# Kernel optimization log

Hardware: AMD Instinct MI355X
Metric: run time of the kernel (lower is better)

Reference implementation:

```python
import jax, jax.numpy as jnp
import numpy as np

B, T, D, H = 4, 2048, 512, 8
K = D // H  # head dim = 64

def setup_inputs() -> dict:
    key = jax.random.key(0)
    k1, k2, k3, k4 = jax.random.split(key, 4)
    x = jax.random.normal(k1, (B, T, D), dtype=jnp.float32)
    # torch nn.Linear stores weight as [out_features, in_features]
    w_qkv = jax.random.normal(k2, (3 * D, D), dtype=jnp.float32) * (D ** -0.5)
    w_proj = jax.random.normal(k3, (D, D), dtype=jnp.float32) * (D ** -0.5)
    b_proj = jax.random.normal(k4, (D,), dtype=jnp.float32) * 0.01
    return {"x": x, "w_qkv": w_qkv, "w_proj": w_proj, "b_proj": b_proj}

def reference(x, w_qkv, w_proj, b_proj):
    Bx, Tx, Dx = x.shape
    # qkv projection (no bias): [B,T,3D]
    qkv = jnp.einsum('btd,ed->bte', x, w_qkv)
    q, k, v = jnp.split(qkv, 3, axis=-1)
    # [B,H,T,K]
    def heads(t):
        return t.reshape(Bx, Tx, H, K).transpose(0, 2, 1, 3)
    q, k, v = heads(q), heads(k), heads(v)
    # scaled scores with causal mask
    scores = jnp.einsum('bhqk,bhsk->bhqs', q, k) * (K ** -0.5)  # [B,H,T,T]
    causal = jnp.tril(jnp.ones((Tx, Tx), dtype=bool))
    scores = jnp.where(causal, scores, -jnp.inf)
    attn = jax.nn.softmax(scores, axis=-1)  # dropout p=0.0 -> identity
    out = jnp.einsum('bhqs,bhsk->bhqk', attn, v)  # [B,H,T,K]
    out = out.transpose(0, 2, 1, 3).reshape(Bx, Tx, Dx)
    out = jnp.einsum('btd,ed->bte', out, w_proj) + b_proj
    return out
```

## Files before the change

### kernel.cpp

```cpp
#include <hip/hip_runtime.h>
#include <hip/hip_bf16.h>


typedef unsigned short u16;
typedef __attribute__((ext_vector_type(8))) __bf16 bf16x8;
typedef __attribute__((ext_vector_type(8))) unsigned short u16x8;
typedef __attribute__((ext_vector_type(4))) float f32x4;
typedef __attribute__((ext_vector_type(4))) unsigned u32x4;

#define DEV static __device__ __forceinline__

DEV void async16(const u16* g, u16* l) {
  __builtin_amdgcn_global_load_lds(
      (const __attribute__((address_space(1))) unsigned int*)g,
      (__attribute__((address_space(3))) unsigned int*)l, 16, 0, 0);
}
DEV u16x8 gld8(const u16* p) { return *(const u16x8*)p; }
DEV void lst8(u16* p, u16x8 v) { *(u16x8*)p = v; }
DEV bf16x8 ldsld8(const u16* p) {
  return __builtin_bit_cast(bf16x8, *(const u16x8*)p);
}
DEV f32x4 mfma16(bf16x8 a, bf16x8 b, f32x4 c) {
  return __builtin_amdgcn_mfma_f32_16x16x32_bf16(a, b, c, 0, 0, 0);
}
DEV u16 f2b(float f) {
  unsigned u = __builtin_bit_cast(unsigned, f);
  u += 0x7FFFu + ((u >> 16) & 1u);
  return (u16)(u >> 16);
}
DEV unsigned pk2(float x, float y) {
  __hip_bfloat162 t = __float22bfloat162_rn(float2{x, y});
  unsigned r;
  __builtin_memcpy(&r, &t, 4);
  return r;
}
DEV u16x8 pack8(f32x4 a, f32x4 b) {
  u32x4 t;
  t[0] = pk2(a[0], a[1]);
  t[1] = pk2(a[2], a[3]);
  t[2] = pk2(b[0], b[1]);
  t[3] = pk2(b[2], b[3]);
  return __builtin_bit_cast(u16x8, t);
}

__global__ void cvt_all(const float* __restrict__ x, const float* __restrict__ wq,
                        u16* __restrict__ xb, u16* __restrict__ wqb) {
  constexpr long NX = 8192L * 512 / 8;
  constexpr long NQ = 1536L * 512 / 8;
  const long i = (long)blockIdx.x * 256 + threadIdx.x;
  if (i < NX) {
    const float* p = x + i * 8;
    *(u16x8*)(xb + i * 8) = pack8(*(const f32x4*)p, *(const f32x4*)(p + 4));
  } else if (i < NX + NQ) {
    const long j = i - NX;
    const float* p = wq + j * 8;
    *(u16x8*)(wqb + j * 8) = pack8(*(const f32x4*)p, *(const f32x4*)(p + 4));
  }
}

__global__ void gemm_bb(const u16* __restrict__ A, const u16* __restrict__ Bt,
                        u16* __restrict__ C, int N, int K) {
  __shared__ __align__(16) u16 As[2][128 * 32];
  __shared__ __align__(16) u16 Bs[2][128 * 32];

  const int t = threadIdx.x, lane = t & 63, w = t >> 6;
  const int lane15 = lane & 15, quad = lane >> 4;
  const int wr = w >> 1, wc = w & 1;

  const int i = blockIdx.x;
  const int rt = (i & 7) | (((i >> 3) & 7) << 3);
  const int ct = i >> 6;
  const long row0 = (long)rt * 128;
  const int col0 = ct * 128;

  const int srow = w * 16 + (lane >> 2);
  const int scol = (lane & 3) * 8;
  const u16* Ag = A + (row0 + srow) * (long)K + scol;
  const u16* Bg = Bt + ((long)col0 + srow) * (long)K + scol;

  f32x4 acc[4][4];
#pragma unroll
  for (int ii = 0; ii < 4; ii++)
#pragma unroll
    for (int j = 0; j < 4; j++) acc[ii][j] = (f32x4)(0.0f);

  for (int k0 = 0; k0 < K; k0 += 64) {
    __syncthreads();
#pragma unroll
    for (int r = 0; r < 2; r++)
#pragma unroll
      for (int hf = 0; hf < 2; hf++) {
        async16(Ag + (long)r * 64 * K + k0 + hf * 32,
                &As[hf][(r * 64 + w * 16) * 32]);
        async16(Bg + (long)r * 64 * K + k0 + hf * 32,
                &Bs[hf][(r * 64 + w * 16) * 32]);
      }
    __syncthreads();

#pragma unroll
    for (int hf = 0; hf < 2; hf++) {
      bf16x8 a[4], b[4];
#pragma unroll
      for (int ii = 0; ii < 4; ii++)
        a[ii] = ldsld8(&As[hf][(wr * 64 + ii * 16 + lane15) * 32 + quad * 8]);
#pragma unroll
      for (int j = 0; j < 4; j++)
        b[j] = ldsld8(&Bs[hf][(wc * 64 + j * 16 + lane15) * 32 + quad * 8]);
#pragma unroll
      for (int ii = 0; ii < 4; ii++)
#pragma unroll
        for (int j = 0; j < 4; j++) acc[ii][j] = mfma16(a[ii], b[j], acc[ii][j]);
    }
  }

#pragma unroll
  for (int ii = 0; ii < 4; ii++)
#pragma unroll
    for (int j = 0; j < 4; j++) {
      const int col = col0 + wc * 64 + j * 16 + lane15;
      const float sc = (col < 512) ? 0.18033688f : 1.0f;
#pragma unroll
      for (int r = 0; r < 4; r++) {
        const long row = row0 + wr * 64 + ii * 16 + quad * 4 + r;
        C[row * (long)N + col] = f2b(acc[ii][j][r] * sc);
      }
    }
}

__global__ void gemm_b64(const u16* __restrict__ A, const float* __restrict__ Bt,
                         const float* __restrict__ bias, float* __restrict__ C,
                         int N, int K) {
  __shared__ __align__(16) u16 As[2][128 * 32];
  __shared__ __align__(16) u16 Bs[2][64 * 32];

  const int t = threadIdx.x, lane = t & 63, w = t >> 6;
  const int lane15 = lane & 15, quad = lane >> 4;
  const int wr = w >> 1, wc = w & 1;

  const int i = blockIdx.x;
  const int rt = (i & 7) | (((i >> 3) & 7) << 3);
  const int ct = i >> 6;
  const long row0 = (long)rt * 128;
  const int col0 = ct * 64;

  const int srow = w * 16 + (lane >> 2);
  const int scol = (lane & 3) * 8;
  const u16* Ag = A + (row0 + srow) * (long)K + scol;

  const int brow = t >> 2, bc = (t & 3) * 16;
  const float* Bg = Bt + (long)(col0 + brow) * K + bc;
  u16* BsD = &Bs[bc >> 5][brow * 32 + (bc & 31)];

  f32x4 acc[4][2];
#pragma unroll
  for (int ii = 0; ii < 4; ii++)
#pragma unroll
    for (int j = 0; j < 2; j++) acc[ii][j] = (f32x4)(0.0f);

  f32x4 q0 = *(const f32x4*)Bg, q1 = *(const f32x4*)(Bg + 4);
  f32x4 q2 = *(const f32x4*)(Bg + 8), q3 = *(const f32x4*)(Bg + 12);

  for (int k0 = 0; k0 < K; k0 += 64) {
    __syncthreads();
#pragma unroll
    for (int r = 0; r < 2; r++)
#pragma unroll
      for (int hf = 0; hf < 2; hf++)
        async16(Ag + (long)r * 64 * K + k0 + hf * 32,
                &As[hf][(r * 64 + w * 16) * 32]);
    lst8(BsD, pack8(q0, q1));
    lst8(BsD + 8, pack8(q2, q3));
    __syncthreads();

    {
      const int kp = (k0 + 64 < K) ? k0 + 64 : k0;
      q0 = *(const f32x4*)(Bg + kp);     q1 = *(const f32x4*)(Bg + kp + 4);
      q2 = *(const f32x4*)(Bg + kp + 8); q3 = *(const f32x4*)(Bg + kp + 12);
    }

#pragma unroll
    for (int hf = 0; hf < 2; hf++) {
      bf16x8 a[4], b[2];
#pragma unroll
      for (int ii = 0; ii < 4; ii++)
        a[ii] = ldsld8(&As[hf][(wr * 64 + ii * 16 + lane15) * 32 + quad * 8]);
#pragma unroll
      for (int j = 0; j < 2; j++)
        b[j] = ldsld8(&Bs[hf][(wc * 32 + j * 16 + lane15) * 32 + quad * 8]);
#pragma unroll
      for (int ii = 0; ii < 4; ii++)
#pragma unroll
        for (int j = 0; j < 2; j++) acc[ii][j] = mfma16(a[ii], b[j], acc[ii][j]);
    }
  }

#pragma unroll
  for (int ii = 0; ii < 4; ii++)
#pragma unroll
    for (int j = 0; j < 2; j++) {
      const int col = col0 + wc * 32 + j * 16 + lane15;
      const float bv = bias[col];
#pragma unroll
      for (int r = 0; r < 4; r++) {
        const long row = row0 + wr * 64 + ii * 16 + quad * 4 + r;
        C[row * (long)N + col] = acc[ii][j][r] + bv;
      }
    }
}

__global__ void attn_v3(const u16* __restrict__ qkv, u16* __restrict__ out) {
  constexpr int T = 2048, LD = 1536;
  __shared__ __align__(16) u16 Ks[64 * 72];
  __shared__ __align__(16) u16 Vt[64 * 72];
  __shared__ __align__(16) u16 Ps[4][16 * 72];

  const int t = threadIdx.x, lane = t & 63, w = t >> 6;
  const int lane15 = lane & 15, quad = lane >> 4;

  const int i = blockIdx.x;
  int qb = i & 31;
  if (i >= 512) qb = 31 - qb;
  const int h = (i >> 5) & 7;
  const int b = (i >> 8) & 3;
  const long base = (long)b * T * LD;

  const u16* gq =
      qkv + base + (long)(qb * 64 + w * 16 + lane15) * LD + h * 64 + quad * 8;
  const bf16x8 qa0 = __builtin_bit_cast(bf16x8, *(const u16x8*)gq);
  const bf16x8 qa1 = __builtin_bit_cast(bf16x8, *(const u16x8*)(gq + 32));

  const int srow = t >> 3, sc8 = (t & 7) * 8;
  const int vs = t >> 2, vd0 = (t & 3) * 16;

  const int nsb = qb + 1;

  u16x8 kr0, kr1, vr0, vr1;
  {
    const u16* gk = qkv + base + (long)srow * LD + 512 + h * 64 + sc8;
    const u16* gv = qkv + base + (long)vs * LD + 1024 + h * 64 + vd0;
    kr0 = gld8(gk); kr1 = gld8(gk + (long)32 * LD);
    vr0 = gld8(gv); vr1 = gld8(gv + 8);
  }

  float lp[4] = {0.0f, 0.0f, 0.0f, 0.0f};
  f32x4 o[4];
#pragma unroll
  for (int j = 0; j < 4; j++) o[j] = (f32x4)(0.0f);

  const int qrow_base = qb * 64 + w * 16 + quad * 4;

  for (int sb = 0; sb < nsb; ++sb) {
    __syncthreads();
    lst8(&Ks[srow * 72 + sc8], kr0);
    lst8(&Ks[(srow + 32) * 72 + sc8], kr1);
#pragma unroll
    for (int ii = 0; ii < 8; ii++) {
      const int d = vd0 + ii;
      Vt[d * 72 + (vs ^ (((d >> 3) & 7) << 3))] = vr0[ii];
    }
#pragma unroll
    for (int ii = 0; ii < 8; ii++) {
      const int d = vd0 + 8 + ii;
      Vt[d * 72 + (vs ^ (((d >> 3) & 7) << 3))] = vr1[ii];
    }
    __syncthreads();

    {
      const int sp = (sb + 1 < nsb) ? sb + 1 : sb;
      const u16* gk = qkv + base + (long)(sp * 64 + srow) * LD + 512 + h * 64 + sc8;
      const u16* gv = qkv + base + (long)(sp * 64 + vs) * LD + 1024 + h * 64 + vd0;
      kr0 = gld8(gk); kr1 = gld8(gk + (long)32 * LD);
      vr0 = gld8(gv); vr1 = gld8(gv + 8);
    }

    f32x4 sf[4];
#pragma unroll
    for (int j = 0; j < 4; j++) {
      f32x4 z = (f32x4)(0.0f);
      z = mfma16(qa0, ldsld8(&Ks[(j * 16 + lane15) * 72 + quad * 8]), z);
      sf[j] = mfma16(qa1, ldsld8(&Ks[(j * 16 + lane15) * 72 + quad * 8 + 32]), z);
    }

    if (sb == qb) {
      const int scol_base = sb * 64 + lane15;
#pragma unroll
      for (int j = 0; j < 4; j++)
#pragma unroll
        for (int r = 0; r < 4; r++) {
          float p = exp2f(sf[j][r]);
          if (scol_base + j * 16 > qrow_base + r) p = 0.0f;
          sf[j][r] = p;
          lp[r] += p;
        }
    } else {
#pragma unroll
      for (int j = 0; j < 4; j++)
#pragma unroll
        for (int r = 0; r < 4; r++) {
          const float p = exp2f(sf[j][r]);
          sf[j][r] = p;
          lp[r] += p;
        }
    }

    u16* myP = Ps[w];
#pragma unroll
    for (int j = 0; j < 4; j++)
#pragma unroll
      for (int r = 0; r < 4; r++)
        myP[(quad * 4 + r) * 72 + j * 16 + lane15] = f2b(sf[j][r]);
    __asm__ __volatile__("" ::: "memory");
    const bf16x8 pa0 = ldsld8(&myP[lane15 * 72 + quad * 8]);
    const bf16x8 pa1 = ldsld8(&myP[lane15 * 72 + quad * 8 + 32]);
    __asm__ __volatile__("" ::: "memory");

#pragma unroll
    for (int j = 0; j < 4; j++) {
      const int d0 = j * 16 + lane15;
      const int swz = ((d0 >> 3) & 7) << 3;
      o[j] = mfma16(pa0, ldsld8(&Vt[d0 * 72 + ((quad * 8) ^ swz)]), o[j]);
      o[j] = mfma16(pa1, ldsld8(&Vt[d0 * 72 + ((quad * 8 + 32) ^ swz)]), o[j]);
    }
  }

#pragma unroll
  for (int off = 1; off < 16; off <<= 1)
#pragma unroll
    for (int r = 0; r < 4; r++) lp[r] += __shfl_xor(lp[r], off);

  const long orow0 = (long)b * T + qb * 64 + w * 16;
  float inv[4];
#pragma unroll
  for (int r = 0; r < 4; r++) inv[r] = 1.0f / lp[r];
#pragma unroll
  for (int j = 0; j < 4; j++)
#pragma unroll
    for (int r = 0; r < 4; r++)
      out[(orow0 + quad * 4 + r) * 512 + h * 64 + j * 16 + lane15] =
          f2b(o[j][r] * inv[r]);
}

extern "C" void kernel_launch(void* const* d_in, const int* in_sizes, int n_in,
                              void* d_out, int out_size, void* d_ws, size_t ws_size,
                              hipStream_t stream) {
  const float* x      = (const float*)d_in[0];
  const float* w_qkv  = (const float*)d_in[1];
  const float* w_proj = (const float*)d_in[2];
  const float* b_proj = (const float*)d_in[3];
  float* out = (float*)d_out;

  u16* qkv = (u16*)d_ws;
  u16* xb  = qkv + (size_t)8192 * 1536;
  u16* wqb = (u16*)d_out;

  cvt_all<<<2432, 256, 0, stream>>>(x, w_qkv, xb, wqb);
  gemm_bb<<<768, 256, 0, stream>>>(xb, wqb, qkv, 1536, 512);
  attn_v3<<<1024, 256, 0, stream>>>(qkv, xb);
  gemm_b64<<<512, 256, 0, stream>>>(xb, w_proj, b_proj, out, 512, 512);
}
```

Baseline: 160.9 us.

## Write V transposed from QKV GEMM epilogue and load it directly in attention

The QKV GEMM epilogue now writes the V third of its output in a transposed [B, head-dim, T] layout using packed 4-element stores, and Q/K go to a separate 1024-wide buffer. The attention kernel then stages V into shared memory with vector stores instead of 16 scalar swizzled transposing stores per thread per tile. P tile writes to shared memory are also packed through pk2. The cost is strided 8-byte global writes in the GEMM epilogue for V, and the V shared-memory reads no longer use the swizzle, which may add bank conflicts.

```diff
diff --git a/kernel.cpp b/kernel.cpp
--- a/kernel.cpp
+++ b/kernel.cpp
@@ -5,8 +5,10 @@
 typedef unsigned short u16;
 typedef __attribute__((ext_vector_type(8))) __bf16 bf16x8;
 typedef __attribute__((ext_vector_type(8))) unsigned short u16x8;
+typedef __attribute__((ext_vector_type(4))) unsigned short u16x4;
 typedef __attribute__((ext_vector_type(4))) float f32x4;
 typedef __attribute__((ext_vector_type(4))) unsigned u32x4;
+typedef __attribute__((ext_vector_type(2))) unsigned u32x2;
 
 #define DEV static __device__ __forceinline__
 
@@ -59,7 +61,7 @@
 }
 
 __global__ void gemm_bb(const u16* __restrict__ A, const u16* __restrict__ Bt,
-                        u16* __restrict__ C, int N, int K) {
+                        u16* __restrict__ qk, u16* __restrict__ vT, int K) {
   __shared__ __align__(16) u16 As[2][128 * 32];
   __shared__ __align__(16) u16 Bs[2][128 * 32];
 
@@ -113,18 +115,35 @@
     }
   }
 
-#pragma unroll
-  for (int ii = 0; ii < 4; ii++)
-#pragma unroll
-    for (int j = 0; j < 4; j++) {
-      const int col = col0 + wc * 64 + j * 16 + lane15;
-      const float sc = (col < 512) ? 0.18033688f : 1.0f;
-#pragma unroll
-      for (int r = 0; r < 4; r++) {
-        const long row = row0 + wr * 64 + ii * 16 + quad * 4 + r;
-        C[row * (long)N + col] = f2b(acc[ii][j][r] * sc);
+  if (col0 >= 1024) {
+#pragma unroll
+    for (int ii = 0; ii < 4; ii++)
+#pragma unroll
+      for (int j = 0; j < 4; j++) {
+        const int hd = col0 - 1024 + wc * 64 + j * 16 + lane15;
+        const long row = row0 + wr * 64 + ii * 16 + quad * 4;
+        const long bb = row >> 11;
+        const int s = (int)(row & 2047);
+        u32x2 pr;
+        pr[0] = pk2(acc[ii][j][0], acc[ii][j][1]);
+        pr[1] = pk2(acc[ii][j][2], acc[ii][j][3]);
+        *(u16x4*)(vT + (bb * 512 + hd) * 2048 + s) =
+            __builtin_bit_cast(u16x4, pr);
       }
-    }
+  } else {
+#pragma unroll
+    for (int ii = 0; ii < 4; ii++)
+#pragma unroll
+      for (int j = 0; j < 4; j++) {
+        const int col = col0 + wc * 64 + j * 16 + lane15;
+        const float sc = (col < 512) ? 0.18033688f : 1.0f;
+#pragma unroll
+        for (int r = 0; r < 4; r++) {
+          const long row = row0 + wr * 64 + ii * 16 + quad * 4 + r;
+          qk[row * 1024 + col] = f2b(acc[ii][j][r] * sc);
+        }
+      }
+  }
 }
 
 __global__ void gemm_b64(const u16* __restrict__ A, const float* __restrict__ Bt,
@@ -208,10 +227,11 @@
     }
 }
 
-__global__ void attn_v3(const u16* __restrict__ qkv, u16* __restrict__ out) {
-  constexpr int T = 2048, LD = 1536;
+__global__ void attn_v6(const u16* __restrict__ qk, const u16* __restrict__ vT,
+                        u16* __restrict__ out) {
+  constexpr int T = 2048, LDQ = 1024;
   __shared__ __align__(16) u16 Ks[64 * 72];
-  __shared__ __align__(16) u16 Vt[64 * 72];
+  __shared__ __align__(16) u16 Vs[64 * 72];
   __shared__ __align__(16) u16 Ps[4][16 * 72];
 
   const int t = threadIdx.x, lane = t & 63, w = t >> 6;
@@ -222,24 +242,24 @@
   if (i >= 512) qb = 31 - qb;
   const int h = (i >> 5) & 7;
   const int b = (i >> 8) & 3;
-  const long base = (long)b * T * LD;
+  const long baseq = (long)b * T * LDQ;
+  const u16* vTb = vT + ((long)b * 512 + h * 64) * 2048;
 
   const u16* gq =
-      qkv + base + (long)(qb * 64 + w * 16 + lane15) * LD + h * 64 + quad * 8;
+      qk + baseq + (long)(qb * 64 + w * 16 + lane15) * LDQ + h * 64 + quad * 8;
   const bf16x8 qa0 = __builtin_bit_cast(bf16x8, *(const u16x8*)gq);
   const bf16x8 qa1 = __builtin_bit_cast(bf16x8, *(const u16x8*)(gq + 32));
 
   const int srow = t >> 3, sc8 = (t & 7) * 8;
-  const int vs = t >> 2, vd0 = (t & 3) * 16;
 
   const int nsb = qb + 1;
 
   u16x8 kr0, kr1, vr0, vr1;
   {
-    const u16* gk = qkv + base + (long)srow * LD + 512 + h * 64 + sc8;
-    const u16* gv = qkv + base + (long)vs * LD + 1024 + h * 64 + vd0;
-    kr0 = gld8(gk); kr1 = gld8(gk + (long)32 * LD);
-    vr0 = gld8(gv); vr1 = gld8(gv + 8);
+    const u16* gk = qk + baseq + (long)srow * LDQ + 512 + h * 64 + sc8;
+    kr0 = gld8(gk); kr1 = gld8(gk + (long)32 * LDQ);
+    const u16* gv = vTb + (long)srow * 2048 + sc8;
+    vr0 = gld8(gv); vr1 = gld8(gv + (long)32 * 2048);
   }
 
   float lp[4] = {0.0f, 0.0f, 0.0f, 0.0f};
@@ -253,24 +273,17 @@
     __syncthreads();
     lst8(&Ks[srow * 72 + sc8], kr0);
     lst8(&Ks[(srow + 32) * 72 + sc8], kr1);
-#pragma unroll
-    for (int ii = 0; ii < 8; ii++) {
-      const int d = vd0 + ii;
-      Vt[d * 72 + (vs ^ (((d >> 3) & 7) << 3))] = vr0[ii];
-    }
-#pragma unroll
-    for (int ii = 0; ii < 8; ii++) {
-      const int d = vd0 + 8 + ii;
-      Vt[d * 72 + (vs ^ (((d >> 3) & 7) << 3))] = vr1[ii];
-    }
+    lst8(&Vs[srow * 72 + sc8], vr0);
+    lst8(&Vs[(srow + 32) * 72 + sc8], vr1);
     __syncthreads();
 
     {
       const int sp = (sb + 1 < nsb) ? sb + 1 : sb;
-      const u16* gk = qkv + base + (long)(sp * 64 + srow) * LD + 512 + h * 64 + sc8;
-      const u16* gv = qkv + base + (long)(sp * 64 + vs) * LD + 1024 + h * 64 + vd0;
-      kr0 = gld8(gk); kr1 = gld8(gk + (long)32 * LD);
-      vr0 = gld8(gv); vr1 = gld8(gv + 8);
+      const u16* gk =
+          qk + baseq + (long)(sp * 64 + srow) * LDQ + 512 + h * 64 + sc8;
+      kr0 = gld8(gk); kr1 = gld8(gk + (long)32 * LDQ);
+      const u16* gv = vTb + (long)srow * 2048 + sp * 64 + sc8;
+      vr0 = gld8(gv); vr1 = gld8(gv + (long)32 * 2048);
     }
 
     f32x4 sf[4];
@@ -305,10 +318,15 @@
 
     u16* myP = Ps[w];
 #pragma unroll
-    for (int j = 0; j < 4; j++)
-#pragma unroll
-      for (int r = 0; r < 4; r++)
-        myP[(quad * 4 + r) * 72 + j * 16 + lane15] = f2b(sf[j][r]);
+    for (int r = 0; r < 4; r++) {
+      const int ro = (quad * 4 + r) * 72 + lane15;
+      const unsigned v01 = pk2(sf[0][r], sf[1][r]);
+      const unsigned v23 = pk2(sf[2][r], sf[3][r]);
+      myP[ro] = (u16)v01;
+      myP[ro + 16] = (u16)(v01 >> 16);
+      myP[ro + 32] = (u16)v23;
+      myP[ro + 48] = (u16)(v23 >> 16);
+    }
     __asm__ __volatile__("" ::: "memory");
     const bf16x8 pa0 = ldsld8(&myP[lane15 * 72 + quad * 8]);
     const bf16x8 pa1 = ldsld8(&myP[lane15 * 72 + quad * 8 + 32]);
@@ -316,10 +334,9 @@
 
 #pragma unroll
     for (int j = 0; j < 4; j++) {
-      const int d0 = j * 16 + lane15;
-      const int swz = ((d0 >> 3) & 7) << 3;
-      o[j] = mfma16(pa0, ldsld8(&Vt[d0 * 72 + ((quad * 8) ^ swz)]), o[j]);
-      o[j] = mfma16(pa1, ldsld8(&Vt[d0 * 72 + ((quad * 8 + 32) ^ swz)]), o[j]);
+      const int d0 = (j * 16 + lane15) * 72;
+      o[j] = mfma16(pa0, ldsld8(&Vs[d0 + quad * 8]), o[j]);
+      o[j] = mfma16(pa1, ldsld8(&Vs[d0 + quad * 8 + 32]), o[j]);
     }
   }
 
@@ -349,12 +366,13 @@
   const float* b_proj = (const float*)d_in[3];
   float* out = (float*)d_out;
 
-  u16* qkv = (u16*)d_ws;
-  u16* xb  = qkv + (size_t)8192 * 1536;
+  u16* qk = (u16*)d_ws;
+  u16* vT = qk + (size_t)8192 * 1024;
+  u16* xb = vT + (size_t)4 * 512 * 2048;
   u16* wqb = (u16*)d_out;
 
   cvt_all<<<2432, 256, 0, stream>>>(x, w_qkv, xb, wqb);
-  gemm_bb<<<768, 256, 0, stream>>>(xb, wqb, qkv, 1536, 512);
-  attn_v3<<<1024, 256, 0, stream>>>(qkv, xb);
+  gemm_bb<<<768, 256, 0, stream>>>(xb, wqb, qk, vT, 512);
+  attn_v6<<<1024, 256, 0, stream>>>(qk, vT, xb);
   gemm_b64<<<512, 256, 0, stream>>>(xb, w_proj, b_proj, out, 512, 512);
 }
```

Result: faster. 153.9 us (-4.4%).
